# Performance work log

Hardware: AMD Instinct MI355X
Metric: run time of the kernel (lower is better)

The kernel has to match this reference:

```python
import jax, jax.numpy as jnp
import numpy as np


def setup_inputs() -> dict:
    key = jax.random.key(0)
    k1, k2, k3 = jax.random.split(key, 3)
    codes = jax.random.normal(k1, (16, 128, 128, 128), dtype=jnp.float32)
    # segmentation map: integer {0,1} component masks, [b, s, 1, h, w]
    segmap = jax.random.randint(k2, (16, 4, 1, 256, 256), 0, 2, dtype=jnp.int32)
    fc_w = jax.random.normal(k3, (512, 128), dtype=jnp.float32) * 0.02
    fc_b = jnp.zeros((512,), dtype=jnp.float32)
    return {"codes": codes, "segmap": segmap, "fc_w": fc_w, "fc_b": fc_b}


def _nearest_resize_2d(x, h_out, w_out):
    # torch F.interpolate(mode='nearest'): in_idx = floor(out_idx * in/out)
    h_in, w_in = x.shape[-2], x.shape[-1]
    hi = jnp.floor(jnp.arange(h_out) * (h_in / h_out)).astype(jnp.int32)
    wi = jnp.floor(jnp.arange(w_out) * (w_in / w_out)).astype(jnp.int32)
    return x[..., hi, :][..., :, wi]


def reference(codes, segmap, fc_w, fc_b):
    # codes: [b, f, h, w]; segmap: [b, s, 1, H, W] int
    b, s = segmap.shape[0], segmap.shape[1]
    H, W = segmap.shape[3], segmap.shape[4]
    seg = segmap.reshape(b, s, H, W)
    h, w = codes.shape[2], codes.shape[3]
    seg = _nearest_resize_2d(seg, h, w)                # [b, s, h, w]
    mask = (seg != 0).astype(codes.dtype)              # [b, s, h, w]
    # fused masked segment-mean: one pass over codes
    sums = jnp.einsum('bfhw,bshw->bsf', codes, mask)   # [b, s, f]
    counts = mask.sum(axis=(2, 3))[..., None]          # [b, s, 1]
    feats = jnp.where(counts > 0, sums / jnp.maximum(counts, 1.0), 0.0)
    return feats @ fc_w.T + fc_b                       # [b, s, 512]
```

## Files before the change

### kernel.cpp

```cpp
#include <hip/hip_runtime.h>

#define B    16
#define S    4
#define F    128
#define HW   16384
#define HWIN 65536
#define OUT  512
#define PBLK 16

__global__ __launch_bounds__(256) void mask_pack_kernel(
    const int* __restrict__ segmap,
    unsigned char* __restrict__ pmask,
    int* __restrict__ pcounts) {
    const int b   = blockIdx.x >> 4;
    const int t   = threadIdx.x;
    const int pbase = (blockIdx.x & 15) * 1024 + t * 4;
    const int y = pbase >> 7;
    const int x = pbase & 127;
    const int* sm = segmap + (size_t)b * (S * HWIN);
    const int row = (2 * y) * 256 + 2 * x;

    unsigned char outb[4] = {0, 0, 0, 0};
    int cnt[S];
#pragma unroll
    for (int s = 0; s < S; ++s) {
        const int4 l0 = *(const int4*)(sm + s * HWIN + row);
        const int4 l1 = *(const int4*)(sm + s * HWIN + row + 4);
        int c = 0;
        if (l0.x) { outb[0] |= (1 << s); c++; }
        if (l0.z) { outb[1] |= (1 << s); c++; }
        if (l1.x) { outb[2] |= (1 << s); c++; }
        if (l1.z) { outb[3] |= (1 << s); c++; }
        cnt[s] = c;
    }
    *(uchar4*)(pmask + (size_t)b * HW + pbase) =
        make_uchar4(outb[0], outb[1], outb[2], outb[3]);

    __shared__ int sc[4][S];
#pragma unroll
    for (int s = 0; s < S; ++s) {
#pragma unroll
        for (int off = 32; off > 0; off >>= 1)
            cnt[s] += __shfl_down(cnt[s], off);
    }
    const int wave = t >> 6;
    if ((t & 63) == 0) {
#pragma unroll
        for (int s = 0; s < S; ++s) sc[wave][s] = cnt[s];
    }
    __syncthreads();
    if (t < S)
        pcounts[blockIdx.x * S + t] = sc[0][t] + sc[1][t] + sc[2][t] + sc[3][t];
}

__global__ __launch_bounds__(256) void masked_sum_kernel(
    const float* __restrict__ codes,
    const unsigned char* __restrict__ pmask,
    float* __restrict__ sums) {
    const int bf = blockIdx.x;
    const int b  = bf >> 7;
    const int t  = threadIdx.x;
    const float4* cp = (const float4*)(codes + (size_t)bf * HW);
    const uchar4* mp = (const uchar4*)(pmask + (size_t)b * HW);

    float a0 = 0.f, a1 = 0.f, a2 = 0.f, a3 = 0.f;
#pragma unroll
    for (int i = 0; i < 8; ++i) {
        const int idx = i * 512 + t;
        const float4 c0 = cp[idx];
        const float4 c1 = cp[idx + 256];
        const uchar4 m0 = mp[idx];
        const uchar4 m1 = mp[idx + 256];
#define ACC(mm, cc)                                \
        {                                          \
            a0 += ((mm) & 1) ? (cc) : 0.f;         \
            a1 += ((mm) & 2) ? (cc) : 0.f;         \
            a2 += ((mm) & 4) ? (cc) : 0.f;         \
            a3 += ((mm) & 8) ? (cc) : 0.f;         \
        }
        ACC(m0.x, c0.x); ACC(m0.y, c0.y); ACC(m0.z, c0.z); ACC(m0.w, c0.w);
        ACC(m1.x, c1.x); ACC(m1.y, c1.y); ACC(m1.z, c1.z); ACC(m1.w, c1.w);
#undef ACC
    }
#pragma unroll
    for (int off = 32; off > 0; off >>= 1) {
        a0 += __shfl_down(a0, off);
        a1 += __shfl_down(a1, off);
        a2 += __shfl_down(a2, off);
        a3 += __shfl_down(a3, off);
    }
    __shared__ float part[4][S];
    const int wave = t >> 6;
    if ((t & 63) == 0) {
        part[wave][0] = a0; part[wave][1] = a1;
        part[wave][2] = a2; part[wave][3] = a3;
    }
    __syncthreads();
    if (t < S) {
        const int f = bf & 127;
        sums[(size_t)(b * S + t) * F + f] =
            part[0][t] + part[1][t] + part[2][t] + part[3][t];
    }
}

__global__ __launch_bounds__(512) void fc_kernel(
    const float* __restrict__ sums,
    const int* __restrict__ pcounts,
    const float* __restrict__ fc_w,
    const float* __restrict__ fc_b,
    float* __restrict__ out) {
    const int bs = blockIdx.x;
    const int b  = bs >> 2;
    const int s  = bs & 3;
    const int t  = threadIdx.x;
    __shared__ float feats[F];
    __shared__ float sinv;
    if (t == 0) {
        int c = 0;
#pragma unroll
        for (int blk = 0; blk < PBLK; ++blk)
            c += pcounts[(b * PBLK + blk) * S + s];
        sinv = (c > 0) ? (1.0f / (float)c) : 0.0f;
    }
    __syncthreads();
    if (t < F) feats[t] = sums[(size_t)bs * F + t] * sinv;
    __syncthreads();

    const float4* w4 = (const float4*)(fc_w + (size_t)t * F);
    const float4* f4 = (const float4*)feats;
    float acc = fc_b[t];
#pragma unroll
    for (int i = 0; i < F / 4; ++i) {
        const float4 wv = w4[i];
        const float4 fv = f4[i];
        acc += fv.x * wv.x + fv.y * wv.y + fv.z * wv.z + fv.w * wv.w;
    }
    out[(size_t)bs * OUT + t] = acc;
}

extern "C" void kernel_launch(void* const* d_in, const int* in_sizes, int n_in,
                              void* d_out, int out_size, void* d_ws, size_t ws_size,
                              hipStream_t stream) {
    const float* codes  = (const float*)d_in[0];
    const int*   segmap = (const int*)d_in[1];
    const float* fc_w   = (const float*)d_in[2];
    const float* fc_b   = (const float*)d_in[3];
    float* out = (float*)d_out;

    unsigned char* pmask = (unsigned char*)d_ws;
    int*   pcounts = (int*)((char*)d_ws + (size_t)B * HW);
    float* sums    = (float*)((char*)d_ws + (size_t)B * HW + B * PBLK * S * 4);

    mask_pack_kernel<<<B * PBLK, 256, 0, stream>>>(segmap, pmask, pcounts);
    masked_sum_kernel<<<B * F, 256, 0, stream>>>(codes, pmask, sums);
    fc_kernel<<<B * S, OUT, 0, stream>>>(sums, pcounts, fc_w, fc_b, out);
}
```

Measured before the change: 218.1 us.

## Fuse FC into masked-sum kernel via last-block atomic counter

Removes the separate FC launch by having the last block finishing each batch's masked sums (tracked with an atomic ready counter reset in the mask-pack kernel) compute the FC for all four segments of that batch. The masked-sum loop is also unrolled to four float4 loads per iteration for more memory-level parallelism. This trades a kernel launch and its dependency gap for atomics, threadfences and a serialized per-batch FC tail.

```diff
diff --git a/kernel.cpp b/kernel.cpp
--- a/kernel.cpp
+++ b/kernel.cpp
@@ -7,13 +7,18 @@
 #define HWIN 65536
 #define OUT  512
 #define PBLK 16
+#define MSBLK 128
 
 __global__ __launch_bounds__(256) void mask_pack_kernel(
     const int* __restrict__ segmap,
     unsigned char* __restrict__ pmask,
-    int* __restrict__ pcounts) {
+    int* __restrict__ pcounts,
+    unsigned int* __restrict__ ready) {
     const int b   = blockIdx.x >> 4;
     const int t   = threadIdx.x;
+    if ((blockIdx.x & 15) == 0 && t == 0)
+        atomicExch(&ready[b], 0u);
+
     const int pbase = (blockIdx.x & 15) * 1024 + t * 4;
     const int y = pbase >> 7;
     const int x = pbase & 127;
@@ -53,10 +58,15 @@
         pcounts[blockIdx.x * S + t] = sc[0][t] + sc[1][t] + sc[2][t] + sc[3][t];
 }
 
-__global__ __launch_bounds__(256) void masked_sum_kernel(
+__global__ __launch_bounds__(256) void masked_sum_fc_kernel(
     const float* __restrict__ codes,
     const unsigned char* __restrict__ pmask,
-    float* __restrict__ sums) {
+    float* __restrict__ sums,
+    const int* __restrict__ pcounts,
+    unsigned int* __restrict__ ready,
+    const float* __restrict__ fc_w,
+    const float* __restrict__ fc_b,
+    float* __restrict__ out) {
     const int bf = blockIdx.x;
     const int b  = bf >> 7;
     const int t  = threadIdx.x;
@@ -65,12 +75,16 @@
 
     float a0 = 0.f, a1 = 0.f, a2 = 0.f, a3 = 0.f;
 #pragma unroll
-    for (int i = 0; i < 8; ++i) {
-        const int idx = i * 512 + t;
+    for (int i = 0; i < 4; ++i) {
+        const int idx = i * 1024 + t;
         const float4 c0 = cp[idx];
         const float4 c1 = cp[idx + 256];
+        const float4 c2 = cp[idx + 512];
+        const float4 c3 = cp[idx + 768];
         const uchar4 m0 = mp[idx];
         const uchar4 m1 = mp[idx + 256];
+        const uchar4 m2 = mp[idx + 512];
+        const uchar4 m3 = mp[idx + 768];
 #define ACC(mm, cc)                                \
         {                                          \
             a0 += ((mm) & 1) ? (cc) : 0.f;         \
@@ -80,6 +94,8 @@
         }
         ACC(m0.x, c0.x); ACC(m0.y, c0.y); ACC(m0.z, c0.z); ACC(m0.w, c0.w);
         ACC(m1.x, c1.x); ACC(m1.y, c1.y); ACC(m1.z, c1.z); ACC(m1.w, c1.w);
+        ACC(m2.x, c2.x); ACC(m2.y, c2.y); ACC(m2.z, c2.z); ACC(m2.w, c2.w);
+        ACC(m3.x, c3.x); ACC(m3.y, c3.y); ACC(m3.z, c3.z); ACC(m3.w, c3.w);
 #undef ACC
     }
 #pragma unroll
@@ -101,41 +117,56 @@
         sums[(size_t)(b * S + t) * F + f] =
             part[0][t] + part[1][t] + part[2][t] + part[3][t];
     }
-}
 
-__global__ __launch_bounds__(512) void fc_kernel(
-    const float* __restrict__ sums,
-    const int* __restrict__ pcounts,
-    const float* __restrict__ fc_w,
-    const float* __restrict__ fc_b,
-    float* __restrict__ out) {
-    const int bs = blockIdx.x;
-    const int b  = bs >> 2;
-    const int s  = bs & 3;
-    const int t  = threadIdx.x;
-    __shared__ float feats[F];
-    __shared__ float sinv;
+    __shared__ int amLast;
     if (t == 0) {
+        __threadfence();
+        const unsigned int old = atomicAdd(&ready[b], 1u);
+        amLast = (old == MSBLK - 1);
+    }
+    __syncthreads();
+    if (!amLast) return;
+    __threadfence();
+
+    __shared__ float feats[S][F];
+    __shared__ float sinv[S];
+    if (t < S) {
         int c = 0;
 #pragma unroll
         for (int blk = 0; blk < PBLK; ++blk)
-            c += pcounts[(b * PBLK + blk) * S + s];
-        sinv = (c > 0) ? (1.0f / (float)c) : 0.0f;
+            c += pcounts[(b * PBLK + blk) * S + t];
+        sinv[t] = (c > 0) ? (1.0f / (float)c) : 0.0f;
     }
     __syncthreads();
-    if (t < F) feats[t] = sums[(size_t)bs * F + t] * sinv;
+    if (t < F) {
+#pragma unroll
+        for (int s = 0; s < S; ++s)
+            feats[s][t] = sums[(size_t)(b * S + s) * F + t] * sinv[s];
+    }
     __syncthreads();
 
-    const float4* w4 = (const float4*)(fc_w + (size_t)t * F);
-    const float4* f4 = (const float4*)feats;
-    float acc = fc_b[t];
+    const float4* w0 = (const float4*)(fc_w + (size_t)t * F);
+    const float4* w1 = (const float4*)(fc_w + (size_t)(t + 256) * F);
+    float acc0[S], acc1[S];
+#pragma unroll
+    for (int s = 0; s < S; ++s) { acc0[s] = fc_b[t]; acc1[s] = fc_b[t + 256]; }
 #pragma unroll
     for (int i = 0; i < F / 4; ++i) {
-        const float4 wv = w4[i];
-        const float4 fv = f4[i];
-        acc += fv.x * wv.x + fv.y * wv.y + fv.z * wv.z + fv.w * wv.w;
+        const float4 wa = w0[i];
+        const float4 wb = w1[i];
+#pragma unroll
+        for (int s = 0; s < S; ++s) {
+            const float4 fv = ((const float4*)feats[s])[i];
+            acc0[s] += fv.x * wa.x + fv.y * wa.y + fv.z * wa.z + fv.w * wa.w;
+            acc1[s] += fv.x * wb.x + fv.y * wb.y + fv.z * wb.z + fv.w * wb.w;
+        }
     }
-    out[(size_t)bs * OUT + t] = acc;
+#pragma unroll
+    for (int s = 0; s < S; ++s) {
+        float* orow = out + (size_t)(b * S + s) * OUT;
+        orow[t]       = acc0[s];
+        orow[t + 256] = acc1[s];
+    }
 }
 
 extern "C" void kernel_launch(void* const* d_in, const int* in_sizes, int n_in,
@@ -147,11 +178,12 @@
     const float* fc_b   = (const float*)d_in[3];
     float* out = (float*)d_out;
 
-    unsigned char* pmask = (unsigned char*)d_ws;
-    int*   pcounts = (int*)((char*)d_ws + (size_t)B * HW);
-    float* sums    = (float*)((char*)d_ws + (size_t)B * HW + B * PBLK * S * 4);
+    unsigned char* pmask   = (unsigned char*)d_ws;
+    int*           pcounts = (int*)((char*)d_ws + (size_t)B * HW);
+    unsigned int*  ready   = (unsigned int*)((char*)pcounts + B * PBLK * S * 4);
+    float*         sums    = (float*)((char*)ready + 256);
 
-    mask_pack_kernel<<<B * PBLK, 256, 0, stream>>>(segmap, pmask, pcounts);
-    masked_sum_kernel<<<B * F, 256, 0, stream>>>(codes, pmask, sums);
-    fc_kernel<<<B * S, OUT, 0, stream>>>(sums, pcounts, fc_w, fc_b, out);
+    mask_pack_kernel<<<B * PBLK, 256, 0, stream>>>(segmap, pmask, pcounts, ready);
+    masked_sum_fc_kernel<<<B * MSBLK, 256, 0, stream>>>(
+        codes, pmask, sums, pcounts, ready, fc_w, fc_b, out);
 }
```

Result: slower. 377.0 us (+72.8%).
